# Performance work log

Hardware: AMD Instinct MI355X
Metric: run time of the kernel (lower is better)

Reference implementation:

```python
import jax, jax.numpy as jnp
import numpy as np

H = 64  # hidden size hard-coded in the torch module


def _lstm_cell(x, h, c, Wih, Whh, b):
    # PyTorch LSTMCell: gates = x @ Wih.T + h @ Whh.T + bias_ih + bias_hh,
    # gate order (i, f, g, o), each of size H.
    gates = x @ Wih.T + h @ Whh.T + b
    i, f, g, o = jnp.split(gates, 4, axis=-1)
    c_new = jax.nn.sigmoid(f) * c + jax.nn.sigmoid(i) * jnp.tanh(g)
    h_new = jax.nn.sigmoid(o) * jnpp_tanh(c_new) if False else jax.nn.sigmoid(o) * jnp.tanh(c_new)
    return h_new, c_new


def setup_inputs() -> dict:
    key = jax.random.key(0)
    ks = jax.random.split(key, 12)
    B, T, F = 2048, 1024, 1
    s = 1.0 / np.sqrt(H)  # PyTorch LSTMCell/Linear init range

    def u(k, shape):
        return jax.random.uniform(k, shape, jnp.float32, -s, s)

    return {
        "input": jax.random.normal(ks[0], (B, T, F), jnp.float32),
        "Wih1": u(ks[1], (4 * H, F)),
        "Whh1": u(ks[2], (4 * H, H)),
        "bih1": u(ks[3], (4 * H,)),
        "bhh1": u(ks[4], (4 * H,)),
        "Wih2": u(ks[5], (4 * H, H)),
        "Whh2": u(ks[6], (4 * H, H)),
        "bih2": u(ks[7], (4 * H,)),
        "bhh2": u(ks[8], (4 * H,)),
        "Wl": u(ks[9], (1, H)),
        "bl": u(ks[10], (1,)),
        "future": 8,
    }


def reference(input, Wih1, Whh1, bih1, bhh1, Wih2, Whh2, bih2, bhh2, Wl, bl, future):
    B = input.shape[0]
    dtype = input.dtype
    z = jnp.zeros((B, H), dtype)
    b1 = bih1 + bhh1
    b2 = bih2 + bhh2

    def step(carry, x_t):
        h1, c1, h2, c2 = carry
        h1, c1 = _lstm_cell(x_t, h1, c1, Wih1, Whh1, b1)
        h2, c2 = _lstm_cell(h1, h2, c2, Wih2, Whh2, b2)
        return (h1, c1, h2, c2), None

    # scan over time: xs shaped [T, B, F]
    (h1, c1, h2, c2), _ = jax.lax.scan(step, (z, z, z, z), jnp.swapaxes(input, 0, 1))
    out = h2 @ Wl.T + bl  # readout from last input step

    def fstep(carry, _):
        out, h1, c1, h2, c2 = carry
        h1, c1 = _lstm_cell(out, h1, c1, Wih1, Whh1, b1)
        h2, c2 = _lstm_cell(h1, h2, c2, Wih2, Whh2, b2)
        out = h2 @ Wl.T + bl
        return (out, h1, c1, h2, c2), None

    (out, h1, c1, h2, c2), _ = jax.lax.scan(fstep, (out, h1, c1, h2, c2), None, length=future)
    return out[:, None, :]  # [B, 1, out_feature]
```

## Files before the change

### kernel.cpp

```cpp
#include <hip/hip_runtime.h>

#define HID 64
#define TSTEPS 1024
#define BPW 8
#define TW 1024

typedef __attribute__((ext_vector_type(8))) short short8v;
typedef __attribute__((ext_vector_type(4))) float f32x4;

__device__ __forceinline__ unsigned short f2bf(float f) {
  unsigned u = __float_as_uint(f);
  u += 0x7FFFu + ((u >> 16) & 1u);
  return (unsigned short)(u >> 16);
}
__device__ __forceinline__ float bf2f(unsigned short h) {
  return __uint_as_float(((unsigned)h) << 16);
}
__device__ __forceinline__ float sigf(float x) {
  return __builtin_amdgcn_rcpf(1.0f + __expf(-x));
}
__device__ __forceinline__ float tanh_(float x) {
  return 1.0f - 2.0f * __builtin_amdgcn_rcpf(1.0f + __expf(2.0f * x));
}
__device__ __forceinline__ float dppror8(float x) {
  int xi = __float_as_int(x);
  int y = __builtin_amdgcn_update_dpp(xi, xi, 0x128, 0xF, 0xF, true);
  return __int_as_float(y);
}
__device__ __forceinline__ f32x4 mf(short8v a, short8v b, f32x4 c) {
  return __builtin_amdgcn_mfma_f32_16x16x32_bf16(a, b, c, 0, 0, 0);
}
__device__ __forceinline__ short8v ld_frag(const short* buf, int ss, int lane) {
  int byte = (ss * 64 + lane) * 16;
  byte ^= ((byte >> 7) & 7) << 4;
  return *(const short8v*)((const char*)buf + byte);
}
__device__ __forceinline__ int frag_addr16(int j, int col) {
  int byte = ((j >> 5) * 64 + ((j & 31) >> 3) * 16 + col) * 16 + (j & 7) * 2;
  byte ^= ((byte >> 7) & 7) << 4;
  return byte;
}
__device__ __forceinline__ void load8split(const float* rp, short8v& hi, short8v& lo) {
  float t[8];
#pragma unroll
  for (int e = 0; e < 8; ++e) t[e] = rp[e];
#pragma unroll
  for (int e = 0; e < 8; ++e) {
    unsigned short h = f2bf(t[e]);
    hi[e] = (short)h;
    lo[e] = (short)f2bf(t[e] - bf2f(h));
  }
}
__device__ __forceinline__ float cellup(float zi, float zf, float zg, float zo,
                                        float& c) {
  c = sigf(zf) * c + sigf(zi) * tanh_(zg);
  return sigf(zo) * tanh_(c);
}

struct __align__(128) SMem {
  float xin[TSTEPS + 1][BPW];
  short hf1[2][1024];
  short hf2[2][1024];
  float ro[8][BPW];
};

#define PINV(v) asm volatile("" : "+v"(v))

__global__ __launch_bounds__(TW, 2) void lstm2_kernel(
    const float* __restrict__ input, const float* __restrict__ Wih1,
    const float* __restrict__ Whh1, const float* __restrict__ bih1,
    const float* __restrict__ bhh1, const float* __restrict__ Wih2,
    const float* __restrict__ Whh2, const float* __restrict__ bih2,
    const float* __restrict__ bhh2, const float* __restrict__ Wl,
    const float* __restrict__ bl, const int* __restrict__ future,
    float* __restrict__ out) {
  __shared__ SMem s;
  const int tid = threadIdx.x;
  const int w = tid >> 6;
  const int lane = tid & 63;
  const int wv = w & 7;
  const bool isL1 = (w < 8);
  const int c = lane & 15;
  const int b = c & 7;
  const int d = (c >> 3) & 1;
  const int g = lane >> 4;
  const int jl = 4 * (2 * wv + d) + g;
  const int b0 = blockIdx.x * BPW;

  short8v WAh[2][2], WAl[2][2], WCh[2][2], WCl[2][2];
  const float* WCsrc = isL1 ? Whh1 : Wih2;
#pragma unroll
  for (int tt = 0; tt < 2; ++tt) {
    const int T = 2 * wv + tt;
    const int r16 = lane & 15;
    const int m = 64 * (r16 & 3) + 4 * T + (r16 >> 2);
    const int koff = (lane >> 4) * 8;
#pragma unroll
    for (int ss = 0; ss < 2; ++ss) {
      load8split(WCsrc + m * HID + ss * 32 + koff, WCh[tt][ss], WCl[tt][ss]);
      load8split(Whh2 + m * HID + ss * 32 + koff, WAh[tt][ss], WAl[tt][ss]);
    }
  }
#pragma unroll
  for (int tt = 0; tt < 2; ++tt)
#pragma unroll
    for (int ss = 0; ss < 2; ++ss) {
      PINV(WAh[tt][ss]); PINV(WAl[tt][ss]);
      PINV(WCh[tt][ss]); PINV(WCl[tt][ss]);
    }

  const float* biA = isL1 ? bih1 : bih2;
  const float* biB = isL1 ? bhh1 : bhh2;
  float bb[4], wi[4];
#pragma unroll
  for (int q = 0; q < 4; ++q) {
    const int row = 64 * q + jl;
    bb[q] = biA[row] + biB[row];
    wi[q] = isL1 ? Wih1[row] : 0.0f;
  }
  const float wlv = isL1 ? 0.0f : Wl[jl];
  const float blv = bl[0];
  const int nfut = future[0];
  const int adr_hi = frag_addr16(jl, b);
  const int adr_lo = frag_addr16(jl, b + 8);

  {
    const float* src = input + (size_t)b0 * TSTEPS;
    for (int idx = tid; idx < BPW * TSTEPS; idx += TW) {
      int bi = idx >> 10;
      int t = idx & (TSTEPS - 1);
      s.xin[t][bi] = src[idx];
    }
    for (int idx = tid; idx < 2 * 1024; idx += TW) {
      ((short*)s.hf1)[idx] = 0;
      ((short*)s.hf2)[idx] = 0;
    }
  }
  const f32x4 zf = (f32x4){0.f, 0.f, 0.f, 0.f};
  f32x4 acc0 = zf, acc1 = zf;
  float cc = 0.f;
  float hnew = 0.f;
  __syncthreads();

  const int total = TSTEPS + nfut;
  for (int sidx = 0; sidx < total; ++sidx) {
    const int p = sidx & 1, pn = p ^ 1;

    if (isL1) {
      float z[4];
#pragma unroll
      for (int q = 0; q < 4; ++q) {
        float z0 = acc0[q] + dppror8(acc0[q]);
        float z1 = acc1[q] + dppror8(acc1[q]);
        z[q] = d ? z1 : z0;
      }
      const int xt = (sidx < TSTEPS) ? sidx : TSTEPS;
      const float xv = s.xin[xt][b];
#pragma unroll
      for (int q = 0; q < 4; ++q) z[q] += bb[q] + xv * wi[q];
      hnew = cellup(z[0], z[1], z[2], z[3], cc);
      unsigned short hh = f2bf(hnew);
      unsigned short hl = f2bf(hnew - bf2f(hh));
      char* hf1w = (char*)s.hf1[pn];
      *(short*)(hf1w + adr_hi) = (short)hh;
      *(short*)(hf1w + adr_lo) = (short)hl;
    } else {
      short8v B0 = ld_frag(s.hf2[p], 0, lane);
      short8v B1 = ld_frag(s.hf2[p], 1, lane);
      acc0 = mf(WAh[0][1], B1,
                mf(WAl[0][1], B1, mf(WAh[0][0], B0, mf(WAl[0][0], B0, zf))));
      acc1 = mf(WAh[1][1], B1,
                mf(WAl[1][1], B1, mf(WAh[1][0], B0, mf(WAl[1][0], B0, zf))));
    }
    __syncthreads();

    {
      short8v C0 = ld_frag(s.hf1[pn], 0, lane);
      short8v C1 = ld_frag(s.hf1[pn], 1, lane);
      if (isL1) {
        acc0 = mf(WCh[0][1], C1,
                  mf(WCl[0][1], C1, mf(WCh[0][0], C0, mf(WCl[0][0], C0, zf))));
        acc1 = mf(WCh[1][1], C1,
                  mf(WCl[1][1], C1, mf(WCh[1][0], C0, mf(WCl[1][0], C0, zf))));
      } else {
        acc0 = mf(WCh[0][1], C1,
                  mf(WCl[0][1], C1, mf(WCh[0][0], C0, mf(WCl[0][0], C0, acc0))));
        acc1 = mf(WCh[1][1], C1,
                  mf(WCl[1][1], C1, mf(WCh[1][0], C0, mf(WCl[1][0], C0, acc1))));
        float z[4];
#pragma unroll
        for (int q = 0; q < 4; ++q) {
          float z0 = acc0[q] + dppror8(acc0[q]);
          float z1 = acc1[q] + dppror8(acc1[q]);
          z[q] = (d ? z1 : z0) + bb[q];
        }
        hnew = cellup(z[0], z[1], z[2], z[3], cc);
        unsigned short hh = f2bf(hnew);
        unsigned short hl = f2bf(hnew - bf2f(hh));
        char* hf2w = (char*)s.hf2[pn];
        *(short*)(hf2w + adr_hi) = (short)hh;
        *(short*)(hf2w + adr_lo) = (short)hl;
      }
    }

    if (sidx >= TSTEPS - 1) {
      if (!isL1) {
        float v = wlv * hnew;
        v += __shfl_xor(v, 8, 64);
        v += __shfl_xor(v, 16, 64);
        v += __shfl_xor(v, 32, 64);
        if (lane < 8) s.ro[wv][lane] = v;
      }
      __syncthreads();
      if (tid < 8) {
        float t = blv;
#pragma unroll
        for (int k = 0; k < 8; ++k) t += s.ro[k][tid];
        s.xin[TSTEPS][tid] = t;
      }
    }
    __syncthreads();
  }

  if (tid < 8) out[b0 + tid] = s.xin[TSTEPS][tid];
}

extern "C" void kernel_launch(void* const* d_in, const int* in_sizes, int n_in,
                              void* d_out, int out_size, void* d_ws,
                              size_t ws_size, hipStream_t stream) {
  const float* input = (const float*)d_in[0];
  const float* Wih1 = (const float*)d_in[1];
  const float* Whh1 = (const float*)d_in[2];
  const float* bih1 = (const float*)d_in[3];
  const float* bhh1 = (const float*)d_in[4];
  const float* Wih2 = (const float*)d_in[5];
  const float* Whh2 = (const float*)d_in[6];
  const float* bih2 = (const float*)d_in[7];
  const float* bhh2 = (const float*)d_in[8];
  const float* Wl = (const float*)d_in[9];
  const float* bl = (const float*)d_in[10];
  const int* fut = (const int*)d_in[11];
  float* out = (float*)d_out;

  const int B = in_sizes[0] / TSTEPS;
  const int blocks = B / BPW;

  hipLaunchKernelGGL(lstm2_kernel, dim3(blocks), dim3(TW), 0, stream, input,
                     Wih1, Whh1, bih1, bhh1, Wih2, Whh2, bih2, bhh2, Wl, bl,
                     fut, out);
}
```

Before: 929.2 us.

## Merge layer-1 and layer-2 waves so each wave computes both LSTM cells

The block shrinks from 16 waves (8 per layer) to 8 waves, each holding all three recurrent weight matrices in registers and computing both layer cells per step. The cross-lane gate fold is reworked to select before a single DPP instead of two, and bf16 rounding now uses the hardware v_cvt_pk_bf16_f32 instruction. The aim is to cut per-step ALU and DPP work and give the two layers' MFMA and elementwise work more room to interleave within a wave. In exchange each wave carries more registers and a longer serial chain per step, and there are fewer waves per block to hide latency.

```diff
diff --git a/kernel.cpp b/kernel.cpp
--- a/kernel.cpp
+++ b/kernel.cpp
@@ -3,7 +3,7 @@
 #define HID 64
 #define TSTEPS 1024
 #define BPW 8
-#define TW 1024
+#define TW 512
 
 typedef __attribute__((ext_vector_type(8))) short short8v;
 typedef __attribute__((ext_vector_type(4))) float f32x4;
@@ -30,6 +30,11 @@
 __device__ __forceinline__ f32x4 mf(short8v a, short8v b, f32x4 c) {
   return __builtin_amdgcn_mfma_f32_16x16x32_bf16(a, b, c, 0, 0, 0);
 }
+__device__ __forceinline__ unsigned cvtpk_bf16(float a) {
+  unsigned r;
+  asm("v_cvt_pk_bf16_f32 %0, %1, %2" : "=v"(r) : "v"(a), "v"(a));
+  return r;
+}
 __device__ __forceinline__ short8v ld_frag(const short* buf, int ss, int lane) {
   int byte = (ss * 64 + lane) * 16;
   byte ^= ((byte >> 7) & 7) << 4;
@@ -55,6 +60,15 @@
                                         float& c) {
   c = sigf(zf) * c + sigf(zi) * tanh_(zg);
   return sigf(zo) * tanh_(c);
+}
+__device__ __forceinline__ void fold2(const f32x4& a0, const f32x4& a1,
+                                      bool dsel, float (&z)[4]) {
+#pragma unroll
+  for (int q = 0; q < 4; ++q) {
+    float send = dsel ? a0[q] : a1[q];
+    float own = dsel ? a1[q] : a0[q];
+    z[q] = own + dppror8(send);
+  }
 }
 
 struct __align__(128) SMem {
@@ -78,47 +92,47 @@
   const int tid = threadIdx.x;
   const int w = tid >> 6;
   const int lane = tid & 63;
-  const int wv = w & 7;
-  const bool isL1 = (w < 8);
   const int c = lane & 15;
   const int b = c & 7;
   const int d = (c >> 3) & 1;
   const int g = lane >> 4;
-  const int jl = 4 * (2 * wv + d) + g;
+  const int jl = 4 * (2 * w + d) + g;
   const int b0 = blockIdx.x * BPW;
 
-  short8v WAh[2][2], WAl[2][2], WCh[2][2], WCl[2][2];
-  const float* WCsrc = isL1 ? Whh1 : Wih2;
+  short8v W1h[2][2], W1l[2][2];
+  short8v W2h[2][2], W2l[2][2];
+  short8v W3h[2][2], W3l[2][2];
 #pragma unroll
   for (int tt = 0; tt < 2; ++tt) {
-    const int T = 2 * wv + tt;
+    const int T = 2 * w + tt;
     const int r16 = lane & 15;
     const int m = 64 * (r16 & 3) + 4 * T + (r16 >> 2);
     const int koff = (lane >> 4) * 8;
 #pragma unroll
     for (int ss = 0; ss < 2; ++ss) {
-      load8split(WCsrc + m * HID + ss * 32 + koff, WCh[tt][ss], WCl[tt][ss]);
-      load8split(Whh2 + m * HID + ss * 32 + koff, WAh[tt][ss], WAl[tt][ss]);
+      load8split(Whh1 + m * HID + ss * 32 + koff, W1h[tt][ss], W1l[tt][ss]);
+      load8split(Wih2 + m * HID + ss * 32 + koff, W2h[tt][ss], W2l[tt][ss]);
+      load8split(Whh2 + m * HID + ss * 32 + koff, W3h[tt][ss], W3l[tt][ss]);
     }
   }
 #pragma unroll
   for (int tt = 0; tt < 2; ++tt)
 #pragma unroll
     for (int ss = 0; ss < 2; ++ss) {
-      PINV(WAh[tt][ss]); PINV(WAl[tt][ss]);
-      PINV(WCh[tt][ss]); PINV(WCl[tt][ss]);
-    }
-
-  const float* biA = isL1 ? bih1 : bih2;
-  const float* biB = isL1 ? bhh1 : bhh2;
-  float bb[4], wi[4];
+      PINV(W1h[tt][ss]); PINV(W1l[tt][ss]);
+      PINV(W2h[tt][ss]); PINV(W2l[tt][ss]);
+      PINV(W3h[tt][ss]); PINV(W3l[tt][ss]);
+    }
+
+  float bb1[4], wi1[4], bb2[4];
 #pragma unroll
   for (int q = 0; q < 4; ++q) {
     const int row = 64 * q + jl;
-    bb[q] = biA[row] + biB[row];
-    wi[q] = isL1 ? Wih1[row] : 0.0f;
-  }
-  const float wlv = isL1 ? 0.0f : Wl[jl];
+    bb1[q] = bih1[row] + bhh1[row];
+    wi1[q] = Wih1[row];
+    bb2[q] = bih2[row] + bhh2[row];
+  }
+  const float wlv = Wl[jl];
   const float blv = bl[0];
   const int nfut = future[0];
   const int adr_hi = frag_addr16(jl, b);
@@ -137,80 +151,71 @@
     }
   }
   const f32x4 zf = (f32x4){0.f, 0.f, 0.f, 0.f};
-  f32x4 acc0 = zf, acc1 = zf;
-  float cc = 0.f;
-  float hnew = 0.f;
+  f32x4 acc1_0 = zf, acc1_1 = zf;
+  f32x4 acc2_0 = zf, acc2_1 = zf;
+  float c1 = 0.f, c2 = 0.f;
+  float h2n = 0.f;
   __syncthreads();
 
   const int total = TSTEPS + nfut;
   for (int sidx = 0; sidx < total; ++sidx) {
     const int p = sidx & 1, pn = p ^ 1;
 
-    if (isL1) {
-      float z[4];
-#pragma unroll
-      for (int q = 0; q < 4; ++q) {
-        float z0 = acc0[q] + dppror8(acc0[q]);
-        float z1 = acc1[q] + dppror8(acc1[q]);
-        z[q] = d ? z1 : z0;
-      }
+    {
+      short8v B0 = ld_frag(s.hf2[p], 0, lane);
+      short8v B1 = ld_frag(s.hf2[p], 1, lane);
+      acc2_0 = mf(W3h[0][1], B1,
+                  mf(W3l[0][1], B1, mf(W3h[0][0], B0, mf(W3l[0][0], B0, zf))));
+      acc2_1 = mf(W3h[1][1], B1,
+                  mf(W3l[1][1], B1, mf(W3h[1][0], B0, mf(W3l[1][0], B0, zf))));
+    }
+    {
       const int xt = (sidx < TSTEPS) ? sidx : TSTEPS;
       const float xv = s.xin[xt][b];
-#pragma unroll
-      for (int q = 0; q < 4; ++q) z[q] += bb[q] + xv * wi[q];
-      hnew = cellup(z[0], z[1], z[2], z[3], cc);
-      unsigned short hh = f2bf(hnew);
-      unsigned short hl = f2bf(hnew - bf2f(hh));
+      float z[4];
+      fold2(acc1_0, acc1_1, d, z);
+#pragma unroll
+      for (int q = 0; q < 4; ++q) z[q] += bb1[q] + xv * wi1[q];
+      float h1n = cellup(z[0], z[1], z[2], z[3], c1);
+      unsigned rh = cvtpk_bf16(h1n);
+      float res = h1n - __uint_as_float(rh << 16);
+      unsigned rl = cvtpk_bf16(res);
       char* hf1w = (char*)s.hf1[pn];
-      *(short*)(hf1w + adr_hi) = (short)hh;
-      *(short*)(hf1w + adr_lo) = (short)hl;
-    } else {
-      short8v B0 = ld_frag(s.hf2[p], 0, lane);
-      short8v B1 = ld_frag(s.hf2[p], 1, lane);
-      acc0 = mf(WAh[0][1], B1,
-                mf(WAl[0][1], B1, mf(WAh[0][0], B0, mf(WAl[0][0], B0, zf))));
-      acc1 = mf(WAh[1][1], B1,
-                mf(WAl[1][1], B1, mf(WAh[1][0], B0, mf(WAl[1][0], B0, zf))));
+      *(short*)(hf1w + adr_hi) = (short)rh;
+      *(short*)(hf1w + adr_lo) = (short)rl;
     }
     __syncthreads();
 
     {
       short8v C0 = ld_frag(s.hf1[pn], 0, lane);
       short8v C1 = ld_frag(s.hf1[pn], 1, lane);
-      if (isL1) {
-        acc0 = mf(WCh[0][1], C1,
-                  mf(WCl[0][1], C1, mf(WCh[0][0], C0, mf(WCl[0][0], C0, zf))));
-        acc1 = mf(WCh[1][1], C1,
-                  mf(WCl[1][1], C1, mf(WCh[1][0], C0, mf(WCl[1][0], C0, zf))));
-      } else {
-        acc0 = mf(WCh[0][1], C1,
-                  mf(WCl[0][1], C1, mf(WCh[0][0], C0, mf(WCl[0][0], C0, acc0))));
-        acc1 = mf(WCh[1][1], C1,
-                  mf(WCl[1][1], C1, mf(WCh[1][0], C0, mf(WCl[1][0], C0, acc1))));
-        float z[4];
-#pragma unroll
-        for (int q = 0; q < 4; ++q) {
-          float z0 = acc0[q] + dppror8(acc0[q]);
-          float z1 = acc1[q] + dppror8(acc1[q]);
-          z[q] = (d ? z1 : z0) + bb[q];
-        }
-        hnew = cellup(z[0], z[1], z[2], z[3], cc);
-        unsigned short hh = f2bf(hnew);
-        unsigned short hl = f2bf(hnew - bf2f(hh));
-        char* hf2w = (char*)s.hf2[pn];
-        *(short*)(hf2w + adr_hi) = (short)hh;
-        *(short*)(hf2w + adr_lo) = (short)hl;
-      }
+      acc2_0 = mf(W2h[0][1], C1,
+                  mf(W2l[0][1], C1, mf(W2h[0][0], C0, mf(W2l[0][0], C0, acc2_0))));
+      acc2_1 = mf(W2h[1][1], C1,
+                  mf(W2l[1][1], C1, mf(W2h[1][0], C0, mf(W2l[1][0], C0, acc2_1))));
+      acc1_0 = mf(W1h[0][1], C1,
+                  mf(W1l[0][1], C1, mf(W1h[0][0], C0, mf(W1l[0][0], C0, zf))));
+      acc1_1 = mf(W1h[1][1], C1,
+                  mf(W1l[1][1], C1, mf(W1h[1][0], C0, mf(W1l[1][0], C0, zf))));
+      float z[4];
+      fold2(acc2_0, acc2_1, d, z);
+#pragma unroll
+      for (int q = 0; q < 4; ++q) z[q] += bb2[q];
+      h2n = cellup(z[0], z[1], z[2], z[3], c2);
+      unsigned rh = cvtpk_bf16(h2n);
+      float res = h2n - __uint_as_float(rh << 16);
+      unsigned rl = cvtpk_bf16(res);
+      char* hf2w = (char*)s.hf2[pn];
+      *(short*)(hf2w + adr_hi) = (short)rh;
+      *(short*)(hf2w + adr_lo) = (short)rl;
     }
 
     if (sidx >= TSTEPS - 1) {
-      if (!isL1) {
-        float v = wlv * hnew;
-        v += __shfl_xor(v, 8, 64);
-        v += __shfl_xor(v, 16, 64);
-        v += __shfl_xor(v, 32, 64);
-        if (lane < 8) s.ro[wv][lane] = v;
-      }
+      float v = wlv * h2n;
+      v += __shfl_xor(v, 8, 64);
+      v += __shfl_xor(v, 16, 64);
+      v += __shfl_xor(v, 32, 64);
+      if (lane < 8) s.ro[w][lane] = v;
       __syncthreads();
       if (tid < 8) {
         float t = blv;
```

Measured after the change: 869.1 us. 1.07x faster.
